# Optimization experiments

Hardware: AMD Instinct MI355X
Metric: run time of the kernel (lower is better)

## Reference

```python
import jax, jax.numpy as jnp
import numpy as np

K = 3  # kernel height/width (filter_size = (1, 3, 3), nF = 9)


def _extract_patches(x):
    """x: [B, C, H, W] -> patches [B, C, H, W, K*K], matching the identity
    grouped conv2d (cross-correlation) with padding=1 in the original:
    patch index i = dy*K + dx corresponds to x[c, h+dy-1, w+dx-1]."""
    B, C, H, W = x.shape
    xp = jnp.pad(x, ((0, 0), (0, 0), (1, 1), (1, 1)))
    # fixed K*K=9 offsets: small static loop, not a data-dim loop
    return jnp.stack(
        [xp[:, :, dy:dy + H, dx:dx + W] for dy in range(K) for dx in range(K)],
        axis=-1,
    )


def setup_inputs() -> dict:
    key = jax.random.key(0)
    k1, k2 = jax.random.split(key)
    B, C, H, W = 4, 128, 180, 320
    nF = K * K
    x = jax.random.normal(k1, (B, C, H, W), dtype=jnp.float32)
    filters = jax.random.normal(k2, (B, nF, H, W), dtype=jnp.float32)
    return {"x": x, "filters": filters}


def reference(x, filters):
    """x: [B, 128, H, W]; filters: [B, 9, H, W]. Returns [B, 128, H, W].
    Equivalent to: im2col (identity grouped conv) then per-pixel matmul
    [128, 9] @ [9, 1] at every spatial location."""
    patches = _extract_patches(x)                       # [B, C, H, W, 9]
    f = jnp.transpose(filters, (0, 2, 3, 1))            # [B, H, W, 9]
    out = jnp.einsum('bchwf,bhwf->bchw', patches, f)    # per-pixel dot
    return out
```

## Files before the change

kernel.cpp:

```cpp
#include <hip/hip_runtime.h>


#define CC 128
#define HH 180
#define WW 320
#define W4 80
#define NF 9
#define CPT 8
#define CQ  (CC / CPT)
#define CST (HH * WW)
#define NTHR (4 * HH * CQ * W4)
#define NBLK (NTHR / 256)
#define XCHUNK (NBLK / 8)

__global__ __launch_bounds__(256, 4) void duf_kernel(
    const float* __restrict__ x,
    const float* __restrict__ f,
    float* __restrict__ out)
{
    int raw = blockIdx.x;
    int wg  = (raw & 7) * XCHUNK + (raw >> 3);
    int n   = wg * 256 + threadIdx.x;

    int w4 = n % W4;
    int t  = n / W4;
    int cq = t % CQ;
    t /= CQ;
    int h  = t % HH;
    int b  = t / HH;

    const float4* f4 = (const float4*)f;
    float4* o4 = (float4*)out;
    const float4 z4 = make_float4(0.f, 0.f, 0.f, 0.f);

    float4 fw[NF];
    size_t fb = ((size_t)(b * NF) * HH + h) * W4 + w4;
#pragma unroll
    for (int i = 0; i < NF; ++i) fw[i] = f4[fb + (size_t)i * (HH * W4)];
    if (h == 0)      { fw[0] = z4; fw[1] = z4; fw[2] = z4; }
    if (h == HH - 1) { fw[6] = z4; fw[7] = z4; fw[8] = z4; }
    if (w4 == 0)     { fw[0].x = 0.f; fw[3].x = 0.f; fw[6].x = 0.f; }
    if (w4 == W4-1)  { fw[2].w = 0.f; fw[5].w = 0.f; fw[8].w = 0.f; }

    const int wB = w4 * 4;
    const int wA = (w4 == 0)      ? wB     : wB - 1;
    const int wC = (w4 == W4 - 1) ? wB + 3 : wB + 4;
    const int r0 = (h == 0)       ? 0      : h - 1;
    const int r2 = (h == HH - 1)  ? HH - 1 : h + 1;
    unsigned orow[3] = { (unsigned)(r0 * WW), (unsigned)(h * WW), (unsigned)(r2 * WW) };
    const unsigned cbase = (unsigned)(b * CC + cq * CPT) * (unsigned)CST;

    float4 Bv[2][3]; float aLv[2][3], cRv[2][3];

#pragma unroll
    for (int r = 0; r < 3; ++r) {
        const float* p = x + (size_t)(cbase + orow[r]);
        Bv[0][r]  = *(const float4*)(p + wB);
        aLv[0][r] = p[wA];
        cRv[0][r] = p[wC];
    }

    size_t ob = ((size_t)(b * CC + cq * CPT) * HH + h) * W4 + w4;

#pragma unroll
    for (int k = 0; k < CPT; ++k) {
        const int cur = k & 1, nxt = cur ^ 1;
        if (k + 1 < CPT) {
            const unsigned cb = cbase + (unsigned)((k + 1) * CST);
#pragma unroll
            for (int r = 0; r < 3; ++r) {
                const float* p = x + (size_t)(cb + orow[r]);
                Bv[nxt][r]  = *(const float4*)(p + wB);
                aLv[nxt][r] = p[wA];
                cRv[nxt][r] = p[wC];
            }
        }
        float4 acc = z4;
#pragma unroll
        for (int r = 0; r < 3; ++r) {
            const float4 f0 = fw[3*r], f1 = fw[3*r+1], f2 = fw[3*r+2];
            const float4 B = Bv[cur][r];
            const float aL = aLv[cur][r], cR = cRv[cur][r];
            acc.x = fmaf(f0.x, aL,  fmaf(f1.x, B.x, fmaf(f2.x, B.y, acc.x)));
            acc.y = fmaf(f0.y, B.x, fmaf(f1.y, B.y, fmaf(f2.y, B.z, acc.y)));
            acc.z = fmaf(f0.z, B.y, fmaf(f1.z, B.z, fmaf(f2.z, B.w, acc.z)));
            acc.w = fmaf(f0.w, B.z, fmaf(f1.w, B.w, fmaf(f2.w, cR,  acc.w)));
        }
        o4[ob + (size_t)k * (HH * W4)] = acc;
    }
}

extern "C" void kernel_launch(void* const* d_in, const int* in_sizes, int n_in,
                              void* d_out, int out_size, void* d_ws, size_t ws_size,
                              hipStream_t stream) {
    const float* x = (const float*)d_in[0];
    const float* f = (const float*)d_in[1];
    float* out = (float*)d_out;
    duf_kernel<<<NBLK, 256, 0, stream>>>(x, f, out);
}
```

Baseline: 256.9 us.

## Replace halo scalar loads with wave shuffles and process 16 channels per thread

Each thread now covers 16 channels of a pixel quad, with blocks ordered so channel groups of the same pixels are adjacent. Left and right halo values come from neighbour lanes via shuffles, and only wave-edge lanes issue extra loads. This cuts redundant scalar global loads and filter reloads. In exchange the explicit double-buffer prefetch is dropped and the channel loop uses a runtime trip count, which may reduce memory-level parallelism.

```diff
diff --git a/kernel.cpp b/kernel.cpp
--- a/kernel.cpp
+++ b/kernel.cpp
@@ -5,88 +5,83 @@
 #define HH 180
 #define WW 320
 #define W4 80
-#define NF 9
-#define CPT 8
-#define CQ  (CC / CPT)
-#define CST (HH * WW)
-#define NTHR (4 * HH * CQ * W4)
-#define NBLK (NTHR / 256)
-#define XCHUNK (NBLK / 8)
+#define PL (HH * W4)
+#define CSPLIT 8
+#define CPG (CC / CSPLIT)
+#define NBLK (4 * PL / 256 * CSPLIT)
 
 __global__ __launch_bounds__(256, 4) void duf_kernel(
     const float* __restrict__ x,
     const float* __restrict__ f,
-    float* __restrict__ out)
+    float* __restrict__ out,
+    int nch)
 {
     int raw = blockIdx.x;
-    int wg  = (raw & 7) * XCHUNK + (raw >> 3);
-    int n   = wg * 256 + threadIdx.x;
+    int pb  = raw >> 3;
+    int cs  = raw & 7;
+    int gp  = pb * 256 + threadIdx.x;
+    int b   = gp / PL;
+    int p   = gp - b * PL;
+    int h   = p / W4;
+    int w4  = p - h * W4;
+    int lane = threadIdx.x & 63;
 
-    int w4 = n % W4;
-    int t  = n / W4;
-    int cq = t % CQ;
-    t /= CQ;
-    int h  = t % HH;
-    int b  = t / HH;
-
-    const float4* f4 = (const float4*)f;
-    float4* o4 = (float4*)out;
+    const float4* f4p = (const float4*)f;
     const float4 z4 = make_float4(0.f, 0.f, 0.f, 0.f);
 
-    float4 fw[NF];
-    size_t fb = ((size_t)(b * NF) * HH + h) * W4 + w4;
+    float4 fw[9];
+    size_t fb = (size_t)(b * 9) * PL + p;
 #pragma unroll
-    for (int i = 0; i < NF; ++i) fw[i] = f4[fb + (size_t)i * (HH * W4)];
+    for (int i = 0; i < 9; ++i) fw[i] = f4p[fb + (size_t)i * PL];
     if (h == 0)      { fw[0] = z4; fw[1] = z4; fw[2] = z4; }
     if (h == HH - 1) { fw[6] = z4; fw[7] = z4; fw[8] = z4; }
     if (w4 == 0)     { fw[0].x = 0.f; fw[3].x = 0.f; fw[6].x = 0.f; }
     if (w4 == W4-1)  { fw[2].w = 0.f; fw[5].w = 0.f; fw[8].w = 0.f; }
 
-    const int wB = w4 * 4;
-    const int wA = (w4 == 0)      ? wB     : wB - 1;
-    const int wC = (w4 == W4 - 1) ? wB + 3 : wB + 4;
-    const int r0 = (h == 0)       ? 0      : h - 1;
-    const int r2 = (h == HH - 1)  ? HH - 1 : h + 1;
-    unsigned orow[3] = { (unsigned)(r0 * WW), (unsigned)(h * WW), (unsigned)(r2 * WW) };
-    const unsigned cbase = (unsigned)(b * CC + cq * CPT) * (unsigned)CST;
+    const int pr0 = (h == 0)      ? p : p - W4;
+    const int pr2 = (h == HH - 1) ? p : p + W4;
+    const bool e0  = (lane == 0);
+    const bool e63 = (lane == 63);
+    const int  eo  = e0 ? -1 : 4;
 
-    float4 Bv[2][3]; float aLv[2][3], cRv[2][3];
+    const size_t cbase = (size_t)(b * CC + cs * CPG) * PL;
+    const float4* xc4 = (const float4*)x + cbase;
+    float4*       oc4 = (float4*)out + cbase;
 
-#pragma unroll
-    for (int r = 0; r < 3; ++r) {
-        const float* p = x + (size_t)(cbase + orow[r]);
-        Bv[0][r]  = *(const float4*)(p + wB);
-        aLv[0][r] = p[wA];
-        cRv[0][r] = p[wC];
-    }
+    for (int k = 0; k < nch; ++k) {
+        const float4* xp = xc4 + (size_t)k * PL;
+        float4 B0 = xp[pr0];
+        float4 B1 = xp[p];
+        float4 B2 = xp[pr2];
+        float g0 = 0.f, g1 = 0.f, g2 = 0.f;
+        if (e0 | e63) {
+            const float* xs = (const float*)xp;
+            g0 = xs[max(4 * pr0 + eo, 0)];
+            g1 = xs[max(4 * p   + eo, 0)];
+            g2 = xs[min(4 * pr2 + eo, 4 * PL - 1)];
+        }
+        float aL0 = __shfl_up(B0.w, 1);  if (e0) aL0 = g0;
+        float aL1 = __shfl_up(B1.w, 1);  if (e0) aL1 = g1;
+        float aL2 = __shfl_up(B2.w, 1);  if (e0) aL2 = g2;
+        float cR0 = __shfl_down(B0.x, 1); if (e63) cR0 = g0;
+        float cR1 = __shfl_down(B1.x, 1); if (e63) cR1 = g1;
+        float cR2 = __shfl_down(B2.x, 1); if (e63) cR2 = g2;
 
-    size_t ob = ((size_t)(b * CC + cq * CPT) * HH + h) * W4 + w4;
+        float4 acc = z4;
+        acc.x = fmaf(fw[0].x, aL0,  fmaf(fw[1].x, B0.x, fmaf(fw[2].x, B0.y, acc.x)));
+        acc.y = fmaf(fw[0].y, B0.x, fmaf(fw[1].y, B0.y, fmaf(fw[2].y, B0.z, acc.y)));
+        acc.z = fmaf(fw[0].z, B0.y, fmaf(fw[1].z, B0.z, fmaf(fw[2].z, B0.w, acc.z)));
+        acc.w = fmaf(fw[0].w, B0.z, fmaf(fw[1].w, B0.w, fmaf(fw[2].w, cR0,  acc.w)));
+        acc.x = fmaf(fw[3].x, aL1,  fmaf(fw[4].x, B1.x, fmaf(fw[5].x, B1.y, acc.x)));
+        acc.y = fmaf(fw[3].y, B1.x, fmaf(fw[4].y, B1.y, fmaf(fw[5].y, B1.z, acc.y)));
+        acc.z = fmaf(fw[3].z, B1.y, fmaf(fw[4].z, B1.z, fmaf(fw[5].z, B1.w, acc.z)));
+        acc.w = fmaf(fw[3].w, B1.z, fmaf(fw[4].w, B1.w, fmaf(fw[5].w, cR1,  acc.w)));
+        acc.x = fmaf(fw[6].x, aL2,  fmaf(fw[7].x, B2.x, fmaf(fw[8].x, B2.y, acc.x)));
+        acc.y = fmaf(fw[6].y, B2.x, fmaf(fw[7].y, B2.y, fmaf(fw[8].y, B2.z, acc.y)));
+        acc.z = fmaf(fw[6].z, B2.y, fmaf(fw[7].z, B2.z, fmaf(fw[8].z, B2.w, acc.z)));
+        acc.w = fmaf(fw[6].w, B2.z, fmaf(fw[7].w, B2.w, fmaf(fw[8].w, cR2,  acc.w)));
 
-#pragma unroll
-    for (int k = 0; k < CPT; ++k) {
-        const int cur = k & 1, nxt = cur ^ 1;
-        if (k + 1 < CPT) {
-            const unsigned cb = cbase + (unsigned)((k + 1) * CST);
-#pragma unroll
-            for (int r = 0; r < 3; ++r) {
-                const float* p = x + (size_t)(cb + orow[r]);
-                Bv[nxt][r]  = *(const float4*)(p + wB);
-                aLv[nxt][r] = p[wA];
-                cRv[nxt][r] = p[wC];
-            }
-        }
-        float4 acc = z4;
-#pragma unroll
-        for (int r = 0; r < 3; ++r) {
-            const float4 f0 = fw[3*r], f1 = fw[3*r+1], f2 = fw[3*r+2];
-            const float4 B = Bv[cur][r];
-            const float aL = aLv[cur][r], cR = cRv[cur][r];
-            acc.x = fmaf(f0.x, aL,  fmaf(f1.x, B.x, fmaf(f2.x, B.y, acc.x)));
-            acc.y = fmaf(f0.y, B.x, fmaf(f1.y, B.y, fmaf(f2.y, B.z, acc.y)));
-            acc.z = fmaf(f0.z, B.y, fmaf(f1.z, B.z, fmaf(f2.z, B.w, acc.z)));
-            acc.w = fmaf(f0.w, B.z, fmaf(f1.w, B.w, fmaf(f2.w, cR,  acc.w)));
-        }
-        o4[ob + (size_t)k * (HH * W4)] = acc;
+        oc4[(size_t)k * PL + p] = acc;
     }
 }
 
@@ -96,5 +91,5 @@
     const float* x = (const float*)d_in[0];
     const float* f = (const float*)d_in[1];
     float* out = (float*)d_out;
-    duf_kernel<<<NBLK, 256, 0, stream>>>(x, f, out);
+    duf_kernel<<<NBLK, 256, 0, stream>>>(x, f, out, CPG);
 }
```

After: 228.0 us. -11.2%, faster.
